# Optimization experiments

Measured on AMD Instinct MI355X. Metric: run time of the kernel, lower is better.

Reference implementation:

```python
import jax, jax.numpy as jnp
import numpy as np
from jax import lax

T = 512
CHUNK = 64
H = W = 28
C = 4
D_MODEL = H * W * C  # 3136
D_HIDDEN = 512
ALPHA = 0.9
ETA0 = 0.1
P = 2.0
EPS = 1e-6


def setup_inputs() -> dict:
    key = jax.random.key(0)
    ks = jax.random.split(key, 8)
    x = jax.random.normal(ks[0], (T, C, H, W), dtype=jnp.float32)
    conv_k_w = jax.random.normal(ks[1], (3, 3, C, C), dtype=jnp.float32) / 6.0  # lecun-ish: fan_in=36
    conv_v_w = jax.random.normal(ks[2], (3, 3, C, C), dtype=jnp.float32) / 6.0
    conv_k_b = jnp.zeros((C,), jnp.float32)
    conv_v_b = jnp.zeros((C,), jnp.float32)
    rms_k_scale = jnp.ones((C,), jnp.float32)
    rms_v_scale = jnp.ones((C,), jnp.float32)
    W1 = jax.random.normal(ks[3], (D_MODEL, D_HIDDEN), dtype=jnp.float32) / np.sqrt(D_MODEL).astype(np.float32)
    b1 = jnp.zeros((D_HIDDEN,), jnp.float32)
    W2 = jax.random.normal(ks[4], (D_HIDDEN, D_MODEL), dtype=jnp.float32) / np.sqrt(D_HIDDEN).astype(np.float32)
    b2 = jnp.zeros((D_MODEL,), jnp.float32)
    return {"x": x, "conv_k_w": conv_k_w, "conv_k_b": conv_k_b,
            "conv_v_w": conv_v_w, "conv_v_b": conv_v_b,
            "rms_k_scale": rms_k_scale, "rms_v_scale": rms_v_scale,
            "W1": W1, "b1": b1, "W2": W2, "b2": b2}


def _conv(x_nhwc, w, b):
    y = lax.conv_general_dilated(x_nhwc, w, window_strides=(1, 1), padding='SAME',
                                 dimension_numbers=('NHWC', 'HWIO', 'NHWC'))
    return y + b


def _rmsnorm(z, scale):
    inv = lax.rsqrt(jnp.mean(z * z, axis=-1, keepdims=True) + EPS)
    return z * inv * scale


def _mlp(params, k):
    w1, bb1, w2, bb2 = params
    return jax.nn.gelu(k @ w1 + bb1) @ w2 + bb2


def reference(x, conv_k_w, conv_k_b, conv_v_w, conv_v_b, rms_k_scale, rms_v_scale, W1, b1, W2, b2):
    t = x.shape[0]
    xh = jnp.transpose(x, (0, 2, 3, 1))  # [T,H,W,C]
    nk = _rmsnorm(_conv(xh, conv_k_w, conv_k_b), rms_k_scale).reshape(t, -1)  # [T, D_MODEL]
    nv = _rmsnorm(_conv(xh, conv_v_w, conv_v_b), rms_v_scale).reshape(t, -1)

    params0 = (W1, b1, W2, b2)

    def loss_per_token(params, k, v):
        pred = _mlp(params, k)
        return jnp.sum(jnp.abs(pred - v) ** P)

    etas = ETA0 * ALPHA ** jnp.arange(CHUNK, dtype=jnp.float32)
    betas = ALPHA ** jnp.arange(CHUNK, dtype=jnp.float32)
    weights = etas * (betas[-1] / betas)  # [CHUNK]

    n_chunks = t // CHUNK
    Kc = nk.reshape(n_chunks, CHUNK, D_MODEL)
    Vc = nv.reshape(n_chunks, CHUNK, D_MODEL)

    def chunk_body(params, kv):
        K, V = kv
        # per-token parameter grads: leaves have leading CHUNK axis
        grads = jax.vmap(jax.grad(loss_per_token), in_axes=(None, 0, 0))(params, K, V)
        new_params = jax.tree.map(
            lambda p, g: p - jnp.tensordot(weights, g, axes=((0,), (0,))), params, grads)
        Y = _mlp(new_params, K)  # recall on keys with updated fast weights
        return new_params, Y

    _, Y_chunks = lax.scan(chunk_body, params0, (Kc, Vc))
    Y = Y_chunks.reshape(t, D_MODEL)
    return Y.reshape(t, C, H, W)
```

## Files before the change

### kernel.cpp

```cpp
#include <hip/hip_runtime.h>
#include <math.h>

#define DM 3136
#define DH 512

typedef __attribute__((ext_vector_type(8))) short bf16x8;
typedef __attribute__((ext_vector_type(4))) float f32x4;

__device__ __forceinline__ ushort f2bf(float f) {
  union { float f; unsigned u; } v; v.f = f;
  unsigned r = v.u + 0x7FFFu + ((v.u >> 16) & 1u);
  return (ushort)(r >> 16);
}

#define MICRO_4x4 \
    acc[0][0] += a.x*b.x; acc[0][1] += a.x*b.y; acc[0][2] += a.x*b.z; acc[0][3] += a.x*b.w; \
    acc[1][0] += a.y*b.x; acc[1][1] += a.y*b.y; acc[1][2] += a.y*b.z; acc[1][3] += a.y*b.w; \
    acc[2][0] += a.z*b.x; acc[2][1] += a.z*b.y; acc[2][2] += a.z*b.z; acc[2][3] += a.z*b.w; \
    acc[3][0] += a.w*b.x; acc[3][1] += a.w*b.y; acc[3][2] += a.w*b.z; acc[3][3] += a.w*b.w;

__device__ __forceinline__ void gelu_both(float xx, float& g, float& gp) {
  const float c = 0.7978845608028654f;
  const float a = 0.044715f;
  float x2 = xx * xx;
  float u = c * (xx + a * xx * x2);
  float t = tanhf(u);
  g  = 0.5f * xx * (1.f + t);
  gp = 0.5f * (1.f + t) + 0.5f * xx * (1.f - t * t) * c * (1.f + 3.f * a * x2);
}
__device__ __forceinline__ float gelu_only(float xx) {
  const float c = 0.7978845608028654f;
  const float a = 0.044715f;
  float u = c * (xx + a * xx * xx * xx);
  return 0.5f * xx * (1.f + tanhf(u));
}

__device__ __forceinline__ void nt64_core(
    const ushort* __restrict__ A, int lda,
    const ushort* __restrict__ B, int ldb,
    int ksteps, f32x4* acc) {
  int lane = threadIdx.x & 63;
  int wv = threadIdx.x >> 6;
  int qr = wv >> 1, qc = wv & 1;
  int lr = lane & 15;
  int lk = (lane >> 4) << 3;
  const ushort* pa0 = A + (size_t)(qr * 32 + lr) * lda + lk;
  const ushort* pa1 = pa0 + (size_t)16 * lda;
  const ushort* pb0 = B + (size_t)(qc * 32 + lr) * ldb + lk;
  const ushort* pb1 = pb0 + (size_t)16 * ldb;
  bf16x8 a0 = *(const bf16x8*)pa0;
  bf16x8 a1 = *(const bf16x8*)pa1;
  bf16x8 b0 = *(const bf16x8*)pb0;
  bf16x8 b1 = *(const bf16x8*)pb1;
  for (int s = 0; s < ksteps; ++s) {
    int sn = (s + 1 < ksteps) ? (s + 1) * 32 : s * 32;
    bf16x8 na0 = *(const bf16x8*)(pa0 + sn);
    bf16x8 na1 = *(const bf16x8*)(pa1 + sn);
    bf16x8 nb0 = *(const bf16x8*)(pb0 + sn);
    bf16x8 nb1 = *(const bf16x8*)(pb1 + sn);
    acc[0] = __builtin_amdgcn_mfma_f32_16x16x32_bf16(a0, b0, acc[0], 0, 0, 0);
    acc[1] = __builtin_amdgcn_mfma_f32_16x16x32_bf16(a0, b1, acc[1], 0, 0, 0);
    acc[2] = __builtin_amdgcn_mfma_f32_16x16x32_bf16(a1, b0, acc[2], 0, 0, 0);
    acc[3] = __builtin_amdgcn_mfma_f32_16x16x32_bf16(a1, b1, acc[3], 0, 0, 0);
    a0 = na0; a1 = na1; b0 = nb0; b1 = nb1;
  }
}

__device__ __forceinline__ void nt64_store(const f32x4* acc, float* __restrict__ dst, int ldc) {
  int lane = threadIdx.x & 63, wv = threadIdx.x >> 6;
  int r0 = (wv >> 1) * 32 + ((lane >> 4) << 2);
  int c0 = (wv & 1) * 32 + (lane & 15);
  #pragma unroll
  for (int r = 0; r < 4; ++r) {
    dst[(size_t)(r0 + r) * ldc + c0]           = acc[0][r];
    dst[(size_t)(r0 + r) * ldc + c0 + 16]      = acc[1][r];
    dst[(size_t)(r0 + r + 16) * ldc + c0]      = acc[2][r];
    dst[(size_t)(r0 + r + 16) * ldc + c0 + 16] = acc[3][r];
  }
}

__global__ __launch_bounds__(256) void conv_rms(
    const float* __restrict__ x,
    const float* __restrict__ wk, const float* __restrict__ bk,
    const float* __restrict__ wv, const float* __restrict__ bv,
    const float* __restrict__ sk, const float* __restrict__ sv,
    const float* __restrict__ W1, ushort* __restrict__ w1tb,
    const float* __restrict__ W2, ushort* __restrict__ W2b0, ushort* __restrict__ W2tb0,
    ushort* __restrict__ nkb, float* __restrict__ nv) {
  __shared__ float smem[4160];
  int tid = threadIdx.x;
  if (blockIdx.x >= 1960) {
    int t = blockIdx.x - 1960;
    int d0 = (t % 49) * 64, h0 = (t / 49) * 64;
    int c = tid & 63, rq = tid >> 6;
    #pragma unroll
    for (int q = 0; q < 16; ++q) {
      int r = q * 4 + rq;
      float v = W2[(size_t)(h0 + r) * DM + d0 + c];
      smem[r * 65 + c] = v;
      W2b0[(size_t)(h0 + r) * DM + d0 + c] = f2bf(v);
    }
    __syncthreads();
    #pragma unroll
    for (int q = 0; q < 16; ++q) {
      int r = q * 4 + rq;
      W2tb0[(size_t)(d0 + r) * DH + h0 + c] = f2bf(smem[c * 65 + r]);
    }
    return;
  }
  if (blockIdx.x >= 1568) {
    int t = blockIdx.x - 1568;
    int d0 = (t % 49) * 64, h0 = (t / 49) * 64;
    int c = tid & 63, rq = tid >> 6;
    #pragma unroll
    for (int q = 0; q < 16; ++q) {
      int r = q * 4 + rq;
      smem[r * 65 + c] = W1[(size_t)(d0 + r) * 512 + h0 + c];
    }
    __syncthreads();
    #pragma unroll
    for (int q = 0; q < 16; ++q) {
      int r = q * 4 + rq;
      w1tb[(size_t)(h0 + r) * 3136 + d0 + c] = f2bf(smem[c * 65 + r]);
    }
    return;
  }
  float* swk = smem;
  float* swv = smem + 144;
  float* sb  = smem + 288;
  if (tid < 144) { swk[tid] = wk[tid]; swv[tid] = wv[tid]; }
  if (tid < 4) {
    sb[tid] = bk[tid]; sb[4 + tid] = bv[tid];
    sb[8 + tid] = sk[tid]; sb[12 + tid] = sv[tid];
  }
  __syncthreads();
  int idx = blockIdx.x * 256 + tid;
  int t = idx / 784, hw = idx - t * 784;
  int h = hw / 28, w = hw - h * 28;
  float ak[4], av[4];
  #pragma unroll
  for (int c = 0; c < 4; ++c) { ak[c] = sb[c]; av[c] = sb[4 + c]; }
  const float* xt = x + (size_t)t * DM;
  for (int kh = 0; kh < 3; ++kh) {
    int ih = h + kh - 1;
    if (ih < 0 || ih >= 28) continue;
    for (int kw = 0; kw < 3; ++kw) {
      int iw = w + kw - 1;
      if (iw < 0 || iw >= 28) continue;
      int base = (kh * 3 + kw) * 16;
      #pragma unroll
      for (int ci = 0; ci < 4; ++ci) {
        float xv = xt[ci * 784 + ih * 28 + iw];
        #pragma unroll
        for (int co = 0; co < 4; ++co) {
          ak[co] += xv * swk[base + ci * 4 + co];
          av[co] += xv * swv[base + ci * 4 + co];
        }
      }
    }
  }
  float mk = (ak[0]*ak[0] + ak[1]*ak[1] + ak[2]*ak[2] + ak[3]*ak[3]) * 0.25f + 1e-6f;
  float mv = (av[0]*av[0] + av[1]*av[1] + av[2]*av[2] + av[3]*av[3]) * 0.25f + 1e-6f;
  float ik = 1.f / sqrtf(mk), iv = 1.f / sqrtf(mv);
  ushort4 ok = { f2bf(ak[0]*ik*sb[8]), f2bf(ak[1]*ik*sb[9]),
                 f2bf(ak[2]*ik*sb[10]), f2bf(ak[3]*ik*sb[11]) };
  float4 ov = { av[0]*iv*sb[12], av[1]*iv*sb[13], av[2]*iv*sb[14], av[3]*iv*sb[15] };
  *(ushort4*)&nkb[(size_t)idx * 4] = ok;
  *(float4*)&nv[(size_t)idx * 4] = ov;
}

__global__ __launch_bounds__(256) void u1_kernel(
    const ushort* __restrict__ nkb, const ushort* __restrict__ w1tb,
    float* __restrict__ KKsl, float* __restrict__ Hb_sl) {
  f32x4 acc[4] = {{0.f,0.f,0.f,0.f},{0.f,0.f,0.f,0.f},{0.f,0.f,0.f,0.f},{0.f,0.f,0.f,0.f}};
  int job = blockIdx.x;
  if (job < 448) {
    int s = job % 7;
    int t = job / 7;
    int m0 = (t >> 3) * 64, n0 = (t & 7) * 64;
    nt64_core(nkb + (size_t)m0 * DM + s * 448, DM, w1tb + (size_t)n0 * DM + s * 448, DM, 14, acc);
    nt64_store(acc, Hb_sl + (size_t)s * 262144 + (size_t)m0 * 512 + n0, 512);
  } else {
    int j2 = job - 448;
    int p = j2 / 7, s = j2 % 7;
    int c = 0;
    while ((c + 1) * (c + 2) / 2 <= p) ++c;
    int j = p - c * (c + 1) / 2;
    nt64_core(nkb + (size_t)c * 64 * DM + s * 448, DM, nkb + (size_t)j * 64 * DM + s * 448, DM, 14, acc);
    nt64_store(acc, KKsl + ((size_t)p * 7 + s) * 4096, 64);
  }
}

__global__ __launch_bounds__(256) void u2_kernel(
    const float* __restrict__ KKsl, const float* __restrict__ Hb_sl,
    float* __restrict__ KKf, float* __restrict__ Hbase,
    const float* __restrict__ b1,
    float* __restrict__ Hh, ushort* __restrict__ Gb, ushort* __restrict__ Gtb,
    float* __restrict__ Gp) {
  int i = blockIdx.x * 256 + threadIdx.x;
  if (i < 147456) {
    int pair = i >> 12, e = i & 4095;
    float s = 0.f;
    #pragma unroll
    for (int t = 0; t < 7; ++t) s += KKsl[((size_t)pair * 7 + t) * 4096 + e];
    KKf[i] = s;
  } else {
    int j = i - 147456;
    float s = 0.f;
    #pragma unroll
    for (int t = 0; t < 7; ++t) s += Hb_sl[(size_t)t * 262144 + j];
    Hbase[j] = s;
    if (j < 32768) {
      Hh[j] = s;
      float g, gp;
      gelu_both(s + b1[j & 511], g, gp);
      Gb[j] = f2bf(g);
      Gtb[(j & 511) * 64 + (j >> 9)] = f2bf(g);
      Gp[j] = gp;
    }
  }
}

__device__ __forceinline__ void hred_body(
    int j, const float* __restrict__ Hb_c, const float* __restrict__ Hcorr, int nsl,
    const float* __restrict__ b1v,
    float* __restrict__ Hh, ushort* __restrict__ Gb, ushort* __restrict__ Gtb,
    float* __restrict__ Gp) {
  float s = Hb_c[j];
  for (int t = 0; t < nsl; ++t) s -= Hcorr[(size_t)t * 32768 + j];
  Hh[j] = s;
  float g, gp;
  gelu_both(s + b1v[j & 511], g, gp);
  Gb[j] = f2bf(g);
  Gtb[(j & 511) * 64 + (j >> 9)] = f2bf(g);
  Gp[j] = gp;
}

__device__ __forceinline__ void hs_corr_job(
    const float* __restrict__ KK, const float* __restrict__ Ewj,
    float* __restrict__ dst, int bx, float* smem) {
  float* As = smem;
  float* Bs = smem + 4096;
  int tid = threadIdx.x;
  int n0 = bx * 64;
  {
    int m = tid >> 2, ib = (tid & 3) * 16;
    #pragma unroll
    for (int q = 0; q < 4; ++q) {
      float4 v = *(const float4*)(KK + m * 64 + ib + q * 4);
      As[(ib + q*4 + 0)*64 + m] = v.x;
      As[(ib + q*4 + 1)*64 + m] = v.y;
      As[(ib + q*4 + 2)*64 + m] = v.z;
      As[(ib + q*4 + 3)*64 + m] = v.w;
    }
    int kr = tid >> 4, nn = (tid & 15) * 4;
    #pragma unroll
    for (int q = 0; q < 4; ++q)
      *(float4*)&Bs[(kr + q*16)*64 + nn] = *(const float4*)(Ewj + (size_t)(kr + q*16) * DH + n0 + nn);
  }
  __syncthreads();
  int tx = tid & 15, ty = tid >> 4;
  float acc[4][4] = {{0.f}};
  #pragma unroll 16
  for (int kk = 0; kk < 64; ++kk) {
    float4 a = *(const float4*)&As[kk*64 + ty * 4];
    float4 b = *(const float4*)&Bs[kk*64 + tx * 4];
    MICRO_4x4
  }
  #pragma unroll
  for (int r = 0; r < 4; ++r) {
    float4 v = { acc[r][0], acc[r][1], acc[r][2], acc[r][3] };
    *(float4*)&dst[(ty*4 + r) * DH + n0 + tx*4] = v;
  }
}

__global__ __launch_bounds__(256) void p4w2_kernel(
    const ushort* __restrict__ Dwb, const ushort* __restrict__ Dwtb,
    const ushort* __restrict__ Gtb, const ushort* __restrict__ W2b_c,
    const float* __restrict__ W2c, float* __restrict__ W2n,
    ushort* __restrict__ W2b_n, ushort* __restrict__ W2tb_n,
    float* __restrict__ Esl) {
  f32x4 acc[4] = {{0.f,0.f,0.f,0.f},{0.f,0.f,0.f,0.f},{0.f,0.f,0.f,0.f},{0.f,0.f,0.f,0.f}};
  int b = blockIdx.x;
  if (b < 56) {
    int s = b % 7, nt = b / 7;
    nt64_core(Dwb + s * 448, DM, W2b_c + (size_t)nt * 64 * DM + s * 448, DM, 14, acc);
    nt64_store(acc, Esl + (size_t)s * 32768 + nt * 64, 512);
  } else {
    int li = b - 56;
    int d0 = (li % 49) * 64, h0 = (li / 49) * 64;
    nt64_core(Gtb + (size_t)h0 * 64, 64, Dwtb + (size_t)d0 * 64, 64, 2, acc);
    int lane = threadIdx.x & 63, wvv = threadIdx.x >> 6;
    int r0 = (wvv >> 1) * 32 + ((lane >> 4) << 2);
    int c0 = (wvv & 1) * 32 + (lane & 15);
    #pragma unroll
    for (int r = 0; r < 4; ++r) {
      #pragma unroll
      for (int p = 0; p < 4; ++p) {
        int h = h0 + r0 + r + ((p >> 1) ? 16 : 0);
        int d = d0 + c0 + ((p & 1) ? 16 : 0);
        size_t off = (size_t)h * DM + d;
        float w = W2c[off] - acc[p][r];
        W2n[off] = w;
        ushort wb = f2bf(w);
        W2b_n[off] = wb;
        W2tb_n[(size_t)d * DH + h] = wb;
      }
    }
  }
}

__global__ __launch_bounds__(256) void g2h_kernel(
    const float* __restrict__ KKf, int ch,
    const float* __restrict__ Esl, const float* __restrict__ GpC,
    const float* __restrict__ Hcur, const float* __restrict__ b1e,
    float* __restrict__ b1o, ushort* __restrict__ G2b,
    float* __restrict__ EwOut, float* __restrict__ Hcorr) {
  __shared__ float smem[8192];
  int blk = blockIdx.x;
  int tid = threadIdx.x;
  int tri = ch * (ch + 1) / 2;
  if (blk < 32) {
    float* KKs = smem;
    float* Ews = smem + 4096;
    float* b1l = smem + 5120;
    const float* KKcc = KKf + (size_t)(tri + ch) * 4096;
    int n0 = blk * 16;
    #pragma unroll
    for (int q = 0; q < 4; ++q) {
      int e4 = q * 256 + tid;
      *(float4*)&KKs[e4 * 4] = *(const float4*)(KKcc + e4 * 4);
    }
    #pragma unroll
    for (int q = 0; q < 4; ++q) {
      int e = q * 256 + tid;
      int i = e >> 4, cc = e & 15;
      size_t off = (size_t)i * 512 + n0 + cc;
      float s = 0.f;
      #pragma unroll
      for (int sl = 0; sl < 7; ++sl) s += Esl[(size_t)sl * 32768 + off];
      Ews[e] = s * GpC[off];
    }
    __syncthreads();
    if (tid < 16) {
      float s = 0.f;
      for (int i = 0; i < 64; ++i) s += Ews[i * 16 + tid];
      b1l[tid] = b1e[n0 + tid] - s;
    }
    __syncthreads();
    #pragma unroll
    for (int q = 0; q < 4; ++q) {
      int e = q * 256 + tid;
      int mrow = e >> 4, cc = e & 15;
      float corr = 0.f;
      #pragma unroll 16
      for (int i = 0; i < 64; ++i) corr += KKs[mrow * 64 + i] * Ews[i * 16 + cc];
      float xx = Hcur[(size_t)mrow * 512 + n0 + cc] - corr + b1l[cc];
      G2b[(size_t)mrow * 512 + n0 + cc] = f2bf(gelu_only(xx));
    }
  } else {
    float* As = smem;
    float* Bs = smem + 4096;
    int bx = blk - 32;
    int n0 = bx * 64;
    #pragma unroll
    for (int q = 0; q < 16; ++q) {
      int e = q * 256 + tid;
      int k = e >> 6, c = e & 63;
      size_t off = (size_t)k * 512 + n0 + c;
      float s = 0.f;
      #pragma unroll
      for (int sl = 0; sl < 7; ++sl) s += Esl[(size_t)sl * 32768 + off];
      float ew = s * GpC[off];
      Bs[k * 64 + c] = ew;
      EwOut[off] = ew;
    }
    {
      const float* KK = KKf + (size_t)((ch + 1) * (ch + 2) / 2 + ch) * 4096;
      int m = tid >> 2, ib = (tid & 3) * 16;
      #pragma unroll
      for (int q = 0; q < 4; ++q) {
        float4 v = *(const float4*)(KK + m * 64 + ib + q * 4);
        As[(ib + q*4 + 0)*64 + m] = v.x;
        As[(ib + q*4 + 1)*64 + m] = v.y;
        As[(ib + q*4 + 2)*64 + m] = v.z;
        As[(ib + q*4 + 3)*64 + m] = v.w;
      }
    }
    __syncthreads();
    if (tid < 64) {
      float s = 0.f;
      for (int k = 0; k < 64; ++k) s += Bs[k * 64 + tid];
      b1o[n0 + tid] = b1e[n0 + tid] - s;
    }
    int tx = tid & 15, ty = tid >> 4;
    float acc[4][4] = {{0.f}};
    #pragma unroll 16
    for (int kk = 0; kk < 64; ++kk) {
      float4 a = *(const float4*)&As[kk*64 + ty * 4];
      float4 b = *(const float4*)&Bs[kk*64 + tx * 4];
      MICRO_4x4
    }
    float* dst = Hcorr + (size_t)ch * 32768;
    #pragma unroll
    for (int r = 0; r < 4; ++r) {
      float4 v = { acc[r][0], acc[r][1], acc[r][2], acc[r][3] };
      *(float4*)&dst[(ty*4 + r) * DH + n0 + tx*4] = v;
    }
  }
}

__global__ __launch_bounds__(256) void p7h_kernel(
    const ushort* __restrict__ G2b, const ushort* __restrict__ W2tb,
    const float* __restrict__ b2n, float* __restrict__ out, int t0,
    const float* __restrict__ Hbase_n, const float* __restrict__ Hcorr, int nsl,
    const float* __restrict__ b1n,
    float* __restrict__ Hh, ushort* __restrict__ Gb_n, ushort* __restrict__ Gtb_n,
    float* __restrict__ Gp) {
  int b = blockIdx.x;
  if (b < 49) {
    f32x4 acc[4] = {{0.f,0.f,0.f,0.f},{0.f,0.f,0.f,0.f},{0.f,0.f,0.f,0.f},{0.f,0.f,0.f,0.f}};
    int n0 = b * 64;
    nt64_core(G2b, 512, W2tb + (size_t)n0 * 512, 512, 16, acc);
    int lane = threadIdx.x & 63, wvv = threadIdx.x >> 6;
    int r0 = (wvv >> 1) * 32 + ((lane >> 4) << 2);
    int c0 = (wvv & 1) * 32 + (lane & 15);
    #pragma unroll
    for (int r = 0; r < 4; ++r) {
      #pragma unroll
      for (int p = 0; p < 4; ++p) {
        int m = r0 + r + ((p >> 1) ? 16 : 0);
        int d = n0 + c0 + ((p & 1) ? 16 : 0);
        out[(size_t)(t0 + m) * DM + d] = acc[p][r] + b2n[d];
      }
    }
  } else {
    int j = (b - 49) * 256 + threadIdx.x;
    hred_body(j, Hbase_n, Hcorr, nsl, b1n, Hh, Gb_n, Gtb_n, Gp);
  }
}

__global__ __launch_bounds__(256) void p3d_kernel(
    const ushort* __restrict__ Gnb, const ushort* __restrict__ W2tb,
    const float* __restrict__ Vn, const float* __restrict__ b2in, float wc2,
    float* __restrict__ b2out, ushort* __restrict__ Dwb, ushort* __restrict__ Dwtb,
    const float* __restrict__ KKf, int ch,
    const float* __restrict__ Ewst, float* __restrict__ Hcorr) {
  __shared__ float smem[8192];
  int blk = blockIdx.x;
  if (blk < 49) {
    f32x4 acc[4] = {{0.f,0.f,0.f,0.f},{0.f,0.f,0.f,0.f},{0.f,0.f,0.f,0.f},{0.f,0.f,0.f,0.f}};
    int n0 = blk * 64;
    nt64_core(Gnb, 512, W2tb + (size_t)n0 * 512, 512, 16, acc);
    int lane = threadIdx.x & 63, wvv = threadIdx.x >> 6;
    int qr = wvv >> 1, qc = wvv & 1;
    int r0 = qr * 32 + ((lane >> 4) << 2);
    int c0 = qc * 32 + (lane & 15);
    float csum[2] = {0.f, 0.f};
    #pragma unroll
    for (int r = 0; r < 4; ++r) {
      #pragma unroll
      for (int p = 0; p < 4; ++p) {
        int m = r0 + r + ((p >> 1) ? 16 : 0);
        int dl = c0 + ((p & 1) ? 16 : 0);
        int d = n0 + dl;
        float dw = wc2 * (acc[p][r] + b2in[d] - Vn[(size_t)m * DM + d]);
        ushort db = f2bf(dw);
        Dwb[(size_t)m * DM + d] = db;
        Dwtb[(size_t)d * 64 + m] = db;
        csum[p & 1] += dw;
      }
    }
    int slot = qr * 4 + ((lane >> 4) & 3);
    smem[(size_t)c0 * 8 + slot] = csum[0];
    smem[(size_t)(c0 + 16) * 8 + slot] = csum[1];
    __syncthreads();
    if (threadIdx.x < 64) {
      float s = 0.f;
      #pragma unroll
      for (int q = 0; q < 8; ++q) s += smem[threadIdx.x * 8 + q];
      b2out[n0 + threadIdx.x] = b2in[n0 + threadIdx.x] - s;
    }
  } else {
    int j2 = blk - 49;
    int j = j2 >> 3, bx = j2 & 7;
    int trin = (ch + 2) * (ch + 3) / 2;
    hs_corr_job(KKf + (size_t)(trin + j) * 4096, Ewst + (size_t)j * 32768,
                Hcorr + (size_t)j * 32768, bx, smem);
  }
}

extern "C" void kernel_launch(void* const* d_in, const int* in_sizes, int n_in,
                              void* d_out, int out_size, void* d_ws, size_t ws_size,
                              hipStream_t stream) {
  const float* x  = (const float*)d_in[0];
  const float* wk = (const float*)d_in[1];
  const float* bk = (const float*)d_in[2];
  const float* wv = (const float*)d_in[3];
  const float* bv = (const float*)d_in[4];
  const float* sk = (const float*)d_in[5];
  const float* sv = (const float*)d_in[6];
  const float* W1 = (const float*)d_in[7];
  const float* b1 = (const float*)d_in[8];
  const float* W2 = (const float*)d_in[9];
  const float* b2 = (const float*)d_in[10];
  float* out = (float*)d_out;
  float* ws  = (float*)d_ws;

  ushort* nkb   = (ushort*)ws;
  ushort* w1tb  = (ushort*)(ws + 802816);
  float* nv     = ws + 1605632;
  float* W2A    = nv + 1605632;
  float* W2B    = W2A + 1605632;
  float* bf_base = W2B + 1605632;
  ushort* W2b0  = (ushort*)bf_base;
  ushort* W2tb0 = (ushort*)(bf_base + 802816);
  ushort* W2bA  = (ushort*)(bf_base + 1605632);
  ushort* W2bB  = (ushort*)(bf_base + 2408448);
  ushort* W2tbA = (ushort*)(bf_base + 3211264);
  ushort* W2tbB = (ushort*)(bf_base + 4014080);
  float* Esl    = bf_base + 4816896;
  float* Hb_sl  = Esl + 229376;
  float* KKsl   = Hb_sl + 1835008;
  float* Hbase  = KKsl + 1032192;
  float* KKf    = Hbase + 262144;
  float* HhA    = KKf + 147456;
  float* HhB    = HhA + 32768;
  float* GpA    = HhB + 32768;
  float* GpB    = GpA + 32768;
  ushort* GbA   = (ushort*)(GpB + 32768);
  ushort* GbB   = (ushort*)(GpB + 49152);
  ushort* GtbA  = (ushort*)(GpB + 65536);
  ushort* GtbB  = (ushort*)(GpB + 81920);
  ushort* G2b   = (ushort*)(GpB + 98304);
  ushort* Dwb   = (ushort*)(GpB + 114688);
  ushort* Dwtb  = (ushort*)(GpB + 215040);
  float* Ewst   = GpB + 315392;
  float* Hcorr  = Ewst + 262144;
  float* b1A    = Hcorr + 229376;
  float* b1B    = b1A + 512;
  float* b2A    = b1B + 512;
  float* b2B    = b2A + 3136;

  float* W2buf[2]   = { W2A, W2B };
  ushort* W2bb[2]   = { W2bA, W2bB };
  ushort* W2tbb[2]  = { W2tbA, W2tbB };
  ushort* Gbb[2]    = { GbA, GbB };
  ushort* Gtbb[2]   = { GtbA, GtbB };
  float* Hhb[2]     = { HhA, HhB };
  float* Gpb[2]     = { GpA, GpB };
  float* b1buf[2]   = { b1A, b1B };
  float* b2buf[2]   = { b2A, b2B };

  float wc2 = 2.0f * (float)(0.1 * pow(0.9, 63.0));

  conv_rms<<<2352, 256, 0, stream>>>(x, wk, bk, wv, bv, sk, sv,
                                     W1, w1tb, W2, W2b0, W2tb0, nkb, nv);
  u1_kernel<<<700, 256, 0, stream>>>(nkb, w1tb, KKsl, Hb_sl);
  u2_kernel<<<1600, 256, 0, stream>>>(KKsl, Hb_sl, KKf, Hbase, b1, HhA, GbA, GtbA, GpA);
  p3d_kernel<<<49, 256, 0, stream>>>(GbA, W2tb0, nv, b2, wc2, b2A, Dwb, Dwtb,
                                     KKf, 0, Ewst, Hcorr);

  for (int ch = 0; ch < 8; ++ch) {
    const float* b1e  = ch ? b1buf[(ch - 1) & 1] : b1;
    const float* W2c  = ch ? W2buf[(ch - 1) & 1] : W2;
    const ushort* W2b_c = ch ? W2bb[(ch - 1) & 1] : W2b0;

    p4w2_kernel<<<448, 256, 0, stream>>>(
        Dwb, Dwtb, Gtbb[ch & 1], W2b_c, W2c,
        W2buf[ch & 1], W2bb[ch & 1], W2tbb[ch & 1], Esl);
    g2h_kernel<<<32 + (ch < 7 ? 8 : 0), 256, 0, stream>>>(
        KKf, ch, Esl, Gpb[ch & 1], Hhb[ch & 1], b1e, b1buf[ch & 1],
        G2b, Ewst + (size_t)ch * 32768, Hcorr);
    p7h_kernel<<<49 + (ch < 7 ? 128 : 0), 256, 0, stream>>>(
        G2b, W2tbb[ch & 1], b2buf[ch & 1], out, ch * 64,
        Hbase + (size_t)((ch + 1) & 7) * 32768, Hcorr, ch + 1, b1buf[ch & 1],
        Hhb[(ch + 1) & 1], Gbb[(ch + 1) & 1], Gtbb[(ch + 1) & 1], Gpb[(ch + 1) & 1]);
    if (ch < 7) {
      int gF = 49 + (ch < 6 ? 8 * (ch + 1) : 0);
      p3d_kernel<<<gF, 256, 0, stream>>>(
          Gbb[(ch + 1) & 1], W2tbb[ch & 1], nv + (size_t)(ch + 1) * 200704,
          b2buf[ch & 1], wc2, b2buf[(ch + 1) & 1], Dwb, Dwtb,
          KKf, ch, Ewst, Hcorr);
    }
  }
}
```

Before: 418.2 us.

## Split K across two wave groups in the 64-column GEMM kernels

The p3d and p7h GEMM paths move to 512-thread blocks. Each 256-thread group computes half of the K=512 reduction, and the two partial results are summed through shared memory, so each block runs more waves to cover latency on a grid of only 49 tiles. A dedicated pred0 kernel replaces the first p3d launch. g2h pads its KK shared tile to a stride of 65 to avoid bank conflicts, and the hred part of p7h now uses 512 threads per block. The cost is an extra shared-memory reduction and barrier, and half of each block sits idle during the epilogue.

```diff
diff --git a/kernel.cpp b/kernel.cpp
--- a/kernel.cpp
+++ b/kernel.cpp
@@ -66,6 +66,58 @@
   }
 }
 
+__device__ __forceinline__ void nt64_group(
+    const ushort* __restrict__ A, int lda,
+    const ushort* __restrict__ B, int ldb,
+    int k0, int ksteps, int lane, int wv, f32x4* acc) {
+  int qr = wv >> 1, qc = wv & 1;
+  int lr = lane & 15;
+  int lk = (lane >> 4) << 3;
+  const ushort* pa0 = A + (size_t)(qr * 32 + lr) * lda + k0 + lk;
+  const ushort* pa1 = pa0 + (size_t)16 * lda;
+  const ushort* pb0 = B + (size_t)(qc * 32 + lr) * ldb + k0 + lk;
+  const ushort* pb1 = pb0 + (size_t)16 * ldb;
+  bf16x8 a0 = *(const bf16x8*)pa0;
+  bf16x8 a1 = *(const bf16x8*)pa1;
+  bf16x8 b0 = *(const bf16x8*)pb0;
+  bf16x8 b1 = *(const bf16x8*)pb1;
+  for (int s = 0; s < ksteps; ++s) {
+    int sn = (s + 1 < ksteps) ? (s + 1) * 32 : s * 32;
+    bf16x8 na0 = *(const bf16x8*)(pa0 + sn);
+    bf16x8 na1 = *(const bf16x8*)(pa1 + sn);
+    bf16x8 nb0 = *(const bf16x8*)(pb0 + sn);
+    bf16x8 nb1 = *(const bf16x8*)(pb1 + sn);
+    acc[0] = __builtin_amdgcn_mfma_f32_16x16x32_bf16(a0, b0, acc[0], 0, 0, 0);
+    acc[1] = __builtin_amdgcn_mfma_f32_16x16x32_bf16(a0, b1, acc[1], 0, 0, 0);
+    acc[2] = __builtin_amdgcn_mfma_f32_16x16x32_bf16(a1, b0, acc[2], 0, 0, 0);
+    acc[3] = __builtin_amdgcn_mfma_f32_16x16x32_bf16(a1, b1, acc[3], 0, 0, 0);
+    a0 = na0; a1 = na1; b0 = nb0; b1 = nb1;
+  }
+}
+
+__device__ __forceinline__ void ksplit_reduce(
+    f32x4* acc, float* red, int grp, int lane, int wv) {
+  int r0 = (wv >> 1) * 32 + ((lane >> 4) << 2);
+  int c0 = (wv & 1) * 32 + (lane & 15);
+  if (grp == 1) {
+    #pragma unroll
+    for (int r = 0; r < 4; ++r) {
+      #pragma unroll
+      for (int p = 0; p < 4; ++p)
+        red[(r0 + r + ((p >> 1) ? 16 : 0)) * 64 + c0 + ((p & 1) ? 16 : 0)] = acc[p][r];
+    }
+  }
+  __syncthreads();
+  if (grp == 0) {
+    #pragma unroll
+    for (int r = 0; r < 4; ++r) {
+      #pragma unroll
+      for (int p = 0; p < 4; ++p)
+        acc[p][r] += red[(r0 + r + ((p >> 1) ? 16 : 0)) * 64 + c0 + ((p & 1) ? 16 : 0)];
+    }
+  }
+}
+
 __device__ __forceinline__ void nt64_store(const f32x4* acc, float* __restrict__ dst, int ldc) {
   int lane = threadIdx.x & 63, wv = threadIdx.x >> 6;
   int r0 = (wv >> 1) * 32 + ((lane >> 4) << 2);
@@ -76,6 +128,44 @@
     dst[(size_t)(r0 + r) * ldc + c0 + 16]      = acc[1][r];
     dst[(size_t)(r0 + r + 16) * ldc + c0]      = acc[2][r];
     dst[(size_t)(r0 + r + 16) * ldc + c0 + 16] = acc[3][r];
+  }
+}
+
+__device__ __forceinline__ void dw_epilogue512(
+    const f32x4* acc, int n0, const float* __restrict__ Vn,
+    const float* __restrict__ b2in, float wc2,
+    ushort* __restrict__ Dwb_o, ushort* __restrict__ Dwt_o,
+    float* __restrict__ b2out, float* smem, int tid) {
+  if (tid < 256) {
+    int lane = tid & 63, wvv = tid >> 6;
+    int qr = wvv >> 1, qc = wvv & 1;
+    int r0 = qr * 32 + ((lane >> 4) << 2);
+    int c0 = qc * 32 + (lane & 15);
+    float csum[2] = {0.f, 0.f};
+    #pragma unroll
+    for (int r = 0; r < 4; ++r) {
+      #pragma unroll
+      for (int p = 0; p < 4; ++p) {
+        int m = r0 + r + ((p >> 1) ? 16 : 0);
+        int dl = c0 + ((p & 1) ? 16 : 0);
+        int d = n0 + dl;
+        float dw = wc2 * (acc[p][r] + b2in[d] - Vn[(size_t)m * DM + d]);
+        ushort db = f2bf(dw);
+        Dwb_o[(size_t)m * DM + d] = db;
+        Dwt_o[(size_t)d * 64 + m] = db;
+        csum[p & 1] += dw;
+      }
+    }
+    int slot = qr * 4 + ((lane >> 4) & 3);
+    smem[(size_t)c0 * 8 + slot] = csum[0];
+    smem[(size_t)(c0 + 16) * 8 + slot] = csum[1];
+  }
+  __syncthreads();
+  if (tid < 64) {
+    float s = 0.f;
+    #pragma unroll
+    for (int q = 0; q < 8; ++q) s += smem[tid * 8 + q];
+    b2out[n0 + tid] = b2in[n0 + tid] - s;
   }
 }
 
@@ -236,29 +326,28 @@
   Gp[j] = gp;
 }
 
-__device__ __forceinline__ void hs_corr_job(
+__device__ __forceinline__ void hs_corr_load(
     const float* __restrict__ KK, const float* __restrict__ Ewj,
-    float* __restrict__ dst, int bx, float* smem) {
-  float* As = smem;
-  float* Bs = smem + 4096;
-  int tid = threadIdx.x;
+    int bx, float* As, float* Bs, int tid) {
   int n0 = bx * 64;
-  {
-    int m = tid >> 2, ib = (tid & 3) * 16;
-    #pragma unroll
-    for (int q = 0; q < 4; ++q) {
-      float4 v = *(const float4*)(KK + m * 64 + ib + q * 4);
-      As[(ib + q*4 + 0)*64 + m] = v.x;
-      As[(ib + q*4 + 1)*64 + m] = v.y;
-      As[(ib + q*4 + 2)*64 + m] = v.z;
-      As[(ib + q*4 + 3)*64 + m] = v.w;
-    }
-    int kr = tid >> 4, nn = (tid & 15) * 4;
-    #pragma unroll
-    for (int q = 0; q < 4; ++q)
-      *(float4*)&Bs[(kr + q*16)*64 + nn] = *(const float4*)(Ewj + (size_t)(kr + q*16) * DH + n0 + nn);
-  }
-  __syncthreads();
+  int m = tid >> 2, ib = (tid & 3) * 16;
+  #pragma unroll
+  for (int q = 0; q < 4; ++q) {
+    float4 v = *(const float4*)(KK + m * 64 + ib + q * 4);
+    As[(ib + q*4 + 0)*64 + m] = v.x;
+    As[(ib + q*4 + 1)*64 + m] = v.y;
+    As[(ib + q*4 + 2)*64 + m] = v.z;
+    As[(ib + q*4 + 3)*64 + m] = v.w;
+  }
+  int kr = tid >> 4, nn = (tid & 15) * 4;
+  #pragma unroll
+  for (int q = 0; q < 4; ++q)
+    *(float4*)&Bs[(kr + q*16)*64 + nn] = *(const float4*)(Ewj + (size_t)(kr + q*16) * DH + n0 + nn);
+}
+
+__device__ __forceinline__ void hs_corr_compute(
+    const float* As, const float* Bs, float* __restrict__ dst, int bx, int tid) {
+  int n0 = bx * 64;
   int tx = tid & 15, ty = tid >> 4;
   float acc[4][4] = {{0.f}};
   #pragma unroll 16
@@ -272,6 +361,21 @@
     float4 v = { acc[r][0], acc[r][1], acc[r][2], acc[r][3] };
     *(float4*)&dst[(ty*4 + r) * DH + n0 + tx*4] = v;
   }
+}
+
+__global__ __launch_bounds__(512) void pred0_kernel(
+    const ushort* __restrict__ Gb0, const ushort* __restrict__ W2tb0,
+    const float* __restrict__ V, const float* __restrict__ b2in, float wc2,
+    float* __restrict__ b2out, ushort* __restrict__ Dwb_o, ushort* __restrict__ Dwt_o) {
+  __shared__ float smem[4608];
+  f32x4 acc[4] = {{0.f,0.f,0.f,0.f},{0.f,0.f,0.f,0.f},{0.f,0.f,0.f,0.f},{0.f,0.f,0.f,0.f}};
+  int tid = threadIdx.x;
+  int grp = tid >> 8, lane = tid & 63, wvv = (tid >> 6) & 3;
+  int n0 = blockIdx.x * 64;
+  nt64_group(Gb0, 512, W2tb0 + (size_t)n0 * 512, 512, grp * 256, 8, lane, wvv, acc);
+  ksplit_reduce(acc, smem, grp, lane, wvv);
+  __syncthreads();
+  dw_epilogue512(acc, n0, V, b2in, wc2, Dwb_o, Dwt_o, b2out, smem + 4096, tid);
 }
 
 __global__ __launch_bounds__(256) void p4w2_kernel(
@@ -316,20 +420,20 @@
     const float* __restrict__ Hcur, const float* __restrict__ b1e,
     float* __restrict__ b1o, ushort* __restrict__ G2b,
     float* __restrict__ EwOut, float* __restrict__ Hcorr) {
-  __shared__ float smem[8192];
+  __shared__ float smem[8320];
   int blk = blockIdx.x;
   int tid = threadIdx.x;
   int tri = ch * (ch + 1) / 2;
   if (blk < 32) {
     float* KKs = smem;
-    float* Ews = smem + 4096;
-    float* b1l = smem + 5120;
+    float* Ews = smem + 4160;
+    float* b1l = smem + 5184;
     const float* KKcc = KKf + (size_t)(tri + ch) * 4096;
     int n0 = blk * 16;
     #pragma unroll
-    for (int q = 0; q < 4; ++q) {
-      int e4 = q * 256 + tid;
-      *(float4*)&KKs[e4 * 4] = *(const float4*)(KKcc + e4 * 4);
+    for (int q = 0; q < 16; ++q) {
+      int e = q * 256 + tid;
+      KKs[(e >> 6) * 65 + (e & 63)] = KKcc[e];
     }
     #pragma unroll
     for (int q = 0; q < 4; ++q) {
@@ -354,7 +458,7 @@
       int mrow = e >> 4, cc = e & 15;
       float corr = 0.f;
       #pragma unroll 16
-      for (int i = 0; i < 64; ++i) corr += KKs[mrow * 64 + i] * Ews[i * 16 + cc];
+      for (int i = 0; i < 64; ++i) corr += KKs[mrow * 65 + i] * Ews[i * 16 + cc];
       float xx = Hcur[(size_t)mrow * 512 + n0 + cc] - corr + b1l[cc];
       G2b[(size_t)mrow * 512 + n0 + cc] = f2bf(gelu_only(xx));
     }
@@ -410,37 +514,42 @@
   }
 }
 
-__global__ __launch_bounds__(256) void p7h_kernel(
+__global__ __launch_bounds__(512) void p7h_kernel(
     const ushort* __restrict__ G2b, const ushort* __restrict__ W2tb,
     const float* __restrict__ b2n, float* __restrict__ out, int t0,
     const float* __restrict__ Hbase_n, const float* __restrict__ Hcorr, int nsl,
     const float* __restrict__ b1n,
     float* __restrict__ Hh, ushort* __restrict__ Gb_n, ushort* __restrict__ Gtb_n,
     float* __restrict__ Gp) {
+  __shared__ float red[4096];
   int b = blockIdx.x;
+  int tid = threadIdx.x;
   if (b < 49) {
     f32x4 acc[4] = {{0.f,0.f,0.f,0.f},{0.f,0.f,0.f,0.f},{0.f,0.f,0.f,0.f},{0.f,0.f,0.f,0.f}};
+    int grp = tid >> 8, lane = tid & 63, wvv = (tid >> 6) & 3;
     int n0 = b * 64;
-    nt64_core(G2b, 512, W2tb + (size_t)n0 * 512, 512, 16, acc);
-    int lane = threadIdx.x & 63, wvv = threadIdx.x >> 6;
-    int r0 = (wvv >> 1) * 32 + ((lane >> 4) << 2);
-    int c0 = (wvv & 1) * 32 + (lane & 15);
-    #pragma unroll
-    for (int r = 0; r < 4; ++r) {
-      #pragma unroll
-      for (int p = 0; p < 4; ++p) {
-        int m = r0 + r + ((p >> 1) ? 16 : 0);
-        int d = n0 + c0 + ((p & 1) ? 16 : 0);
-        out[(size_t)(t0 + m) * DM + d] = acc[p][r] + b2n[d];
+    nt64_group(G2b, 512, W2tb + (size_t)n0 * 512, 512, grp * 256, 8, lane, wvv, acc);
+    ksplit_reduce(acc, red, grp, lane, wvv);
+    if (grp == 0) {
+      int r0 = (wvv >> 1) * 32 + ((lane >> 4) << 2);
+      int c0 = (wvv & 1) * 32 + (lane & 15);
+      #pragma unroll
+      for (int r = 0; r < 4; ++r) {
+        #pragma unroll
+        for (int p = 0; p < 4; ++p) {
+          int m = r0 + r + ((p >> 1) ? 16 : 0);
+          int d = n0 + c0 + ((p & 1) ? 16 : 0);
+          out[(size_t)(t0 + m) * DM + d] = acc[p][r] + b2n[d];
+        }
       }
     }
   } else {
-    int j = (b - 49) * 256 + threadIdx.x;
+    int j = (b - 49) * 512 + tid;
     hred_body(j, Hbase_n, Hcorr, nsl, b1n, Hh, Gb_n, Gtb_n, Gp);
   }
 }
 
-__global__ __launch_bounds__(256) void p3d_kernel(
+__global__ __launch_bounds__(512) void p3d_kernel(
     const ushort* __restrict__ Gnb, const ushort* __restrict__ W2tb,
     const float* __restrict__ Vn, const float* __restrict__ b2in, float wc2,
     float* __restrict__ b2out, ushort* __restrict__ Dwb, ushort* __restrict__ Dwtb,
@@ -448,45 +557,25 @@
     const float* __restrict__ Ewst, float* __restrict__ Hcorr) {
   __shared__ float smem[8192];
   int blk = blockIdx.x;
+  int tid = threadIdx.x;
   if (blk < 49) {
     f32x4 acc[4] = {{0.f,0.f,0.f,0.f},{0.f,0.f,0.f,0.f},{0.f,0.f,0.f,0.f},{0.f,0.f,0.f,0.f}};
+    int grp = tid >> 8, lane = tid & 63, wvv = (tid >> 6) & 3;
     int n0 = blk * 64;
-    nt64_core(Gnb, 512, W2tb + (size_t)n0 * 512, 512, 16, acc);
-    int lane = threadIdx.x & 63, wvv = threadIdx.x >> 6;
-    int qr = wvv >> 1, qc = wvv & 1;
-    int r0 = qr * 32 + ((lane >> 4) << 2);
-    int c0 = qc * 32 + (lane & 15);
-    float csum[2] = {0.f, 0.f};
-    #pragma unroll
-    for (int r = 0; r < 4; ++r) {
-      #pragma unroll
-      for (int p = 0; p < 4; ++p) {
-        int m = r0 + r + ((p >> 1) ? 16 : 0);
-        int dl = c0 + ((p & 1) ? 16 : 0);
-        int d = n0 + dl;
-        float dw = wc2 * (acc[p][r] + b2in[d] - Vn[(size_t)m * DM + d]);
-        ushort db = f2bf(dw);
-        Dwb[(size_t)m * DM + d] = db;
-        Dwtb[(size_t)d * 64 + m] = db;
-        csum[p & 1] += dw;
-      }
-    }
-    int slot = qr * 4 + ((lane >> 4) & 3);
-    smem[(size_t)c0 * 8 + slot] = csum[0];
-    smem[(size_t)(c0 + 16) * 8 + slot] = csum[1];
+    nt64_group(Gnb, 512, W2tb + (size_t)n0 * 512, 512, grp * 256, 8, lane, wvv, acc);
+    ksplit_reduce(acc, smem, grp, lane, wvv);
     __syncthreads();
-    if (threadIdx.x < 64) {
-      float s = 0.f;
-      #pragma unroll
-      for (int q = 0; q < 8; ++q) s += smem[threadIdx.x * 8 + q];
-      b2out[n0 + threadIdx.x] = b2in[n0 + threadIdx.x] - s;
-    }
+    dw_epilogue512(acc, n0, Vn, b2in, wc2, Dwb, Dwtb, b2out, smem + 4096, tid);
   } else {
     int j2 = blk - 49;
     int j = j2 >> 3, bx = j2 & 7;
     int trin = (ch + 2) * (ch + 3) / 2;
-    hs_corr_job(KKf + (size_t)(trin + j) * 4096, Ewst + (size_t)j * 32768,
-                Hcorr + (size_t)j * 32768, bx, smem);
+    const float* KK = KKf + (size_t)(trin + j) * 4096;
+    const float* Ewj = Ewst + (size_t)j * 32768;
+    float* dst = Hcorr + (size_t)j * 32768;
+    if (tid < 256) hs_corr_load(KK, Ewj, bx, smem, smem + 4096, tid);
+    __syncthreads();
+    if (tid < 256) hs_corr_compute(smem, smem + 4096, dst, bx, tid);
   }
 }
 
@@ -558,8 +647,7 @@
                                      W1, w1tb, W2, W2b0, W2tb0, nkb, nv);
   u1_kernel<<<700, 256, 0, stream>>>(nkb, w1tb, KKsl, Hb_sl);
   u2_kernel<<<1600, 256, 0, stream>>>(KKsl, Hb_sl, KKf, Hbase, b1, HhA, GbA, GtbA, GpA);
-  p3d_kernel<<<49, 256, 0, stream>>>(GbA, W2tb0, nv, b2, wc2, b2A, Dwb, Dwtb,
-                                     KKf, 0, Ewst, Hcorr);
+  pred0_kernel<<<49, 512, 0, stream>>>(GbA, W2tb0, nv, b2, wc2, b2A, Dwb, Dwtb);
 
   for (int ch = 0; ch < 8; ++ch) {
     const float* b1e  = ch ? b1buf[(ch - 1) & 1] : b1;
@@ -572,13 +660,13 @@
     g2h_kernel<<<32 + (ch < 7 ? 8 : 0), 256, 0, stream>>>(
         KKf, ch, Esl, Gpb[ch & 1], Hhb[ch & 1], b1e, b1buf[ch & 1],
         G2b, Ewst + (size_t)ch * 32768, Hcorr);
-    p7h_kernel<<<49 + (ch < 7 ? 128 : 0), 256, 0, stream>>>(
+    p7h_kernel<<<49 + (ch < 7 ? 64 : 0), 512, 0, stream>>>(
         G2b, W2tbb[ch & 1], b2buf[ch & 1], out, ch * 64,
         Hbase + (size_t)((ch + 1) & 7) * 32768, Hcorr, ch + 1, b1buf[ch & 1],
         Hhb[(ch + 1) & 1], Gbb[(ch + 1) & 1], Gtbb[(ch + 1) & 1], Gpb[(ch + 1) & 1]);
     if (ch < 7) {
       int gF = 49 + (ch < 6 ? 8 * (ch + 1) : 0);
-      p3d_kernel<<<gF, 256, 0, stream>>>(
+      p3d_kernel<<<gF, 512, 0, stream>>>(
           Gbb[(ch + 1) & 1], W2tbb[ch & 1], nv + (size_t)(ch + 1) * 200704,
           b2buf[ch & 1], wc2, b2buf[(ch + 1) & 1], Dwb, Dwtb,
           KKf, ch, Ewst, Hcorr);
```

After: 441.0 us. 5.4% more time.

## Fuse next-chunk hidden reduction into g2h and merge p7h with p3d

Applied to the files above, without the earlier changes.

The next chunk's hidden-state correction (KK×Ew) is now computed inline in g2hr blocks, together with the Hcorr reduction and GELU. Previously it was a separate matmul written to Hcorr and then reduced in p7h. The recall output and the next chunk's prediction/Dw epilogue now share one kernel (yp3), removing one launch per chunk and a global round trip of the Hcorr slice. KK shared tiles are padded to a stride of 65 to avoid bank conflicts. In exchange, g2hr recomputes the Esl reduction in 128 extra blocks, and the work across dependent stages is rebalanced.

```diff
diff --git a/kernel.cpp b/kernel.cpp
--- a/kernel.cpp
+++ b/kernel.cpp
@@ -79,6 +79,42 @@
   }
 }
 
+__device__ __forceinline__ void dw_epilogue256(
+    const f32x4* acc, int n0, const float* __restrict__ Vn,
+    const float* __restrict__ b2in, float wc2,
+    ushort* __restrict__ Dwb_o, ushort* __restrict__ Dwt_o,
+    float* __restrict__ b2out, float* smem) {
+  int lane = threadIdx.x & 63, wvv = threadIdx.x >> 6;
+  int qr = wvv >> 1, qc = wvv & 1;
+  int r0 = qr * 32 + ((lane >> 4) << 2);
+  int c0 = qc * 32 + (lane & 15);
+  float csum[2] = {0.f, 0.f};
+  #pragma unroll
+  for (int r = 0; r < 4; ++r) {
+    #pragma unroll
+    for (int p = 0; p < 4; ++p) {
+      int m = r0 + r + ((p >> 1) ? 16 : 0);
+      int dl = c0 + ((p & 1) ? 16 : 0);
+      int d = n0 + dl;
+      float dw = wc2 * (acc[p][r] + b2in[d] - Vn[(size_t)m * DM + d]);
+      ushort db = f2bf(dw);
+      Dwb_o[(size_t)m * DM + d] = db;
+      Dwt_o[(size_t)d * 64 + m] = db;
+      csum[p & 1] += dw;
+    }
+  }
+  int slot = qr * 4 + ((lane >> 4) & 3);
+  smem[(size_t)c0 * 8 + slot] = csum[0];
+  smem[(size_t)(c0 + 16) * 8 + slot] = csum[1];
+  __syncthreads();
+  if (threadIdx.x < 64) {
+    float s = 0.f;
+    #pragma unroll
+    for (int q = 0; q < 8; ++q) s += smem[threadIdx.x * 8 + q];
+    b2out[n0 + threadIdx.x] = b2in[n0 + threadIdx.x] - s;
+  }
+}
+
 __global__ __launch_bounds__(256) void conv_rms(
     const float* __restrict__ x,
     const float* __restrict__ wk, const float* __restrict__ bk,
@@ -221,21 +257,6 @@
   }
 }
 
-__device__ __forceinline__ void hred_body(
-    int j, const float* __restrict__ Hb_c, const float* __restrict__ Hcorr, int nsl,
-    const float* __restrict__ b1v,
-    float* __restrict__ Hh, ushort* __restrict__ Gb, ushort* __restrict__ Gtb,
-    float* __restrict__ Gp) {
-  float s = Hb_c[j];
-  for (int t = 0; t < nsl; ++t) s -= Hcorr[(size_t)t * 32768 + j];
-  Hh[j] = s;
-  float g, gp;
-  gelu_both(s + b1v[j & 511], g, gp);
-  Gb[j] = f2bf(g);
-  Gtb[(j & 511) * 64 + (j >> 9)] = f2bf(g);
-  Gp[j] = gp;
-}
-
 __device__ __forceinline__ void hs_corr_job(
     const float* __restrict__ KK, const float* __restrict__ Ewj,
     float* __restrict__ dst, int bx, float* smem) {
@@ -272,6 +293,17 @@
     float4 v = { acc[r][0], acc[r][1], acc[r][2], acc[r][3] };
     *(float4*)&dst[(ty*4 + r) * DH + n0 + tx*4] = v;
   }
+}
+
+__global__ __launch_bounds__(256) void pred0_kernel(
+    const ushort* __restrict__ Gb0, const ushort* __restrict__ W2tb0,
+    const float* __restrict__ V, const float* __restrict__ b2in, float wc2,
+    float* __restrict__ b2out, ushort* __restrict__ Dwb_o, ushort* __restrict__ Dwt_o) {
+  __shared__ float smem[512];
+  f32x4 acc[4] = {{0.f,0.f,0.f,0.f},{0.f,0.f,0.f,0.f},{0.f,0.f,0.f,0.f},{0.f,0.f,0.f,0.f}};
+  int n0 = blockIdx.x * 64;
+  nt64_core(Gb0, 512, W2tb0 + (size_t)n0 * 512, 512, 16, acc);
+  dw_epilogue256(acc, n0, V, b2in, wc2, Dwb_o, Dwt_o, b2out, smem);
 }
 
 __global__ __launch_bounds__(256) void p4w2_kernel(
@@ -310,26 +342,28 @@
   }
 }
 
-__global__ __launch_bounds__(256) void g2h_kernel(
+__global__ __launch_bounds__(256) void g2hr_kernel(
     const float* __restrict__ KKf, int ch,
     const float* __restrict__ Esl, const float* __restrict__ GpC,
     const float* __restrict__ Hcur, const float* __restrict__ b1e,
-    float* __restrict__ b1o, ushort* __restrict__ G2b,
-    float* __restrict__ EwOut, float* __restrict__ Hcorr) {
-  __shared__ float smem[8192];
+    float* __restrict__ b1o, ushort* __restrict__ G2b, float* __restrict__ EwOut,
+    const float* __restrict__ Hcorr, const float* __restrict__ Hbase_n,
+    float* __restrict__ HhN, ushort* __restrict__ GbN,
+    ushort* __restrict__ GtbN, float* __restrict__ GpN) {
+  __shared__ float smem[5200];
   int blk = blockIdx.x;
   int tid = threadIdx.x;
   int tri = ch * (ch + 1) / 2;
   if (blk < 32) {
     float* KKs = smem;
-    float* Ews = smem + 4096;
-    float* b1l = smem + 5120;
+    float* Ews = smem + 4160;
+    float* b1l = smem + 5184;
     const float* KKcc = KKf + (size_t)(tri + ch) * 4096;
     int n0 = blk * 16;
     #pragma unroll
-    for (int q = 0; q < 4; ++q) {
-      int e4 = q * 256 + tid;
-      *(float4*)&KKs[e4 * 4] = *(const float4*)(KKcc + e4 * 4);
+    for (int q = 0; q < 16; ++q) {
+      int e = q * 256 + tid;
+      KKs[(e >> 6) * 65 + (e & 63)] = KKcc[e];
     }
     #pragma unroll
     for (int q = 0; q < 4; ++q) {
@@ -354,13 +388,12 @@
       int mrow = e >> 4, cc = e & 15;
       float corr = 0.f;
       #pragma unroll 16
-      for (int i = 0; i < 64; ++i) corr += KKs[mrow * 64 + i] * Ews[i * 16 + cc];
+      for (int i = 0; i < 64; ++i) corr += KKs[mrow * 65 + i] * Ews[i * 16 + cc];
       float xx = Hcur[(size_t)mrow * 512 + n0 + cc] - corr + b1l[cc];
       G2b[(size_t)mrow * 512 + n0 + cc] = f2bf(gelu_only(xx));
     }
-  } else {
-    float* As = smem;
-    float* Bs = smem + 4096;
+  } else if (blk < 40) {
+    float* Bs = smem;
     int bx = blk - 32;
     int n0 = bx * 64;
     #pragma unroll
@@ -375,48 +408,68 @@
       Bs[k * 64 + c] = ew;
       EwOut[off] = ew;
     }
-    {
-      const float* KK = KKf + (size_t)((ch + 1) * (ch + 2) / 2 + ch) * 4096;
-      int m = tid >> 2, ib = (tid & 3) * 16;
-      #pragma unroll
-      for (int q = 0; q < 4; ++q) {
-        float4 v = *(const float4*)(KK + m * 64 + ib + q * 4);
-        As[(ib + q*4 + 0)*64 + m] = v.x;
-        As[(ib + q*4 + 1)*64 + m] = v.y;
-        As[(ib + q*4 + 2)*64 + m] = v.z;
-        As[(ib + q*4 + 3)*64 + m] = v.w;
-      }
-    }
     __syncthreads();
     if (tid < 64) {
       float s = 0.f;
       for (int k = 0; k < 64; ++k) s += Bs[k * 64 + tid];
       b1o[n0 + tid] = b1e[n0 + tid] - s;
     }
-    int tx = tid & 15, ty = tid >> 4;
-    float acc[4][4] = {{0.f}};
+  } else {
+    float* Ewt = smem;
+    float* KKs = smem + 1024;
+    float* b1l = smem + 2064;
+    int bh = blk - 40;
+    int m0 = (bh >> 5) * 16;
+    int c0 = (bh & 31) * 16;
+    #pragma unroll
+    for (int q = 0; q < 4; ++q) {
+      int e = q * 256 + tid;
+      int i = e >> 4, cl = e & 15;
+      size_t off = (size_t)i * 512 + c0 + cl;
+      float s = 0.f;
+      #pragma unroll
+      for (int sl = 0; sl < 7; ++sl) s += Esl[(size_t)sl * 32768 + off];
+      Ewt[i * 16 + cl] = s * GpC[off];
+    }
+    const float* KK = KKf + (size_t)((ch + 1) * (ch + 2) / 2 + ch) * 4096;
+    #pragma unroll
+    for (int q = 0; q < 4; ++q) {
+      int e = q * 256 + tid;
+      int ml = e >> 6, i = e & 63;
+      KKs[ml * 65 + i] = KK[(m0 + ml) * 64 + i];
+    }
+    __syncthreads();
+    if (tid < 16) {
+      float s = 0.f;
+      for (int i = 0; i < 64; ++i) s += Ewt[i * 16 + tid];
+      b1l[tid] = b1e[c0 + tid] - s;
+    }
+    __syncthreads();
+    int ml = tid >> 4, cl = tid & 15;
+    int m = m0 + ml, c = c0 + cl;
+    float corr = 0.f;
     #pragma unroll 16
-    for (int kk = 0; kk < 64; ++kk) {
-      float4 a = *(const float4*)&As[kk*64 + ty * 4];
-      float4 b = *(const float4*)&Bs[kk*64 + tx * 4];
-      MICRO_4x4
-    }
-    float* dst = Hcorr + (size_t)ch * 32768;
-    #pragma unroll
-    for (int r = 0; r < 4; ++r) {
-      float4 v = { acc[r][0], acc[r][1], acc[r][2], acc[r][3] };
-      *(float4*)&dst[(ty*4 + r) * DH + n0 + tx*4] = v;
-    }
-  }
-}
-
-__global__ __launch_bounds__(256) void p7h_kernel(
+    for (int i = 0; i < 64; ++i) corr += KKs[ml * 65 + i] * Ewt[i * 16 + cl];
+    size_t off = (size_t)m * 512 + c;
+    float s = Hbase_n[off] - corr;
+    for (int j = 0; j < ch; ++j) s -= Hcorr[(size_t)j * 32768 + off];
+    HhN[off] = s;
+    float g, gp;
+    gelu_both(s + b1l[cl], g, gp);
+    GbN[off] = f2bf(g);
+    GtbN[(size_t)c * 64 + m] = f2bf(g);
+    GpN[off] = gp;
+  }
+}
+
+__global__ __launch_bounds__(256) void yp3_kernel(
     const ushort* __restrict__ G2b, const ushort* __restrict__ W2tb,
     const float* __restrict__ b2n, float* __restrict__ out, int t0,
-    const float* __restrict__ Hbase_n, const float* __restrict__ Hcorr, int nsl,
-    const float* __restrict__ b1n,
-    float* __restrict__ Hh, ushort* __restrict__ Gb_n, ushort* __restrict__ Gtb_n,
-    float* __restrict__ Gp) {
+    const ushort* __restrict__ Gnb, const float* __restrict__ Vn, float wc2,
+    float* __restrict__ b2out, ushort* __restrict__ Dwb, ushort* __restrict__ Dwtb,
+    const float* __restrict__ KKf, int ch,
+    const float* __restrict__ Ewst, float* __restrict__ Hcorr) {
+  __shared__ float smem[8192];
   int b = blockIdx.x;
   if (b < 49) {
     f32x4 acc[4] = {{0.f,0.f,0.f,0.f},{0.f,0.f,0.f,0.f},{0.f,0.f,0.f,0.f},{0.f,0.f,0.f,0.f}};
@@ -434,55 +487,13 @@
         out[(size_t)(t0 + m) * DM + d] = acc[p][r] + b2n[d];
       }
     }
+  } else if (ch < 7 && b < 98) {
+    f32x4 acc[4] = {{0.f,0.f,0.f,0.f},{0.f,0.f,0.f,0.f},{0.f,0.f,0.f,0.f},{0.f,0.f,0.f,0.f}};
+    int n0 = (b - 49) * 64;
+    nt64_core(Gnb, 512, W2tb + (size_t)n0 * 512, 512, 16, acc);
+    dw_epilogue256(acc, n0, Vn, b2n, wc2, Dwb, Dwtb, b2out, smem);
   } else {
-    int j = (b - 49) * 256 + threadIdx.x;
-    hred_body(j, Hbase_n, Hcorr, nsl, b1n, Hh, Gb_n, Gtb_n, Gp);
-  }
-}
-
-__global__ __launch_bounds__(256) void p3d_kernel(
-    const ushort* __restrict__ Gnb, const ushort* __restrict__ W2tb,
-    const float* __restrict__ Vn, const float* __restrict__ b2in, float wc2,
-    float* __restrict__ b2out, ushort* __restrict__ Dwb, ushort* __restrict__ Dwtb,
-    const float* __restrict__ KKf, int ch,
-    const float* __restrict__ Ewst, float* __restrict__ Hcorr) {
-  __shared__ float smem[8192];
-  int blk = blockIdx.x;
-  if (blk < 49) {
-    f32x4 acc[4] = {{0.f,0.f,0.f,0.f},{0.f,0.f,0.f,0.f},{0.f,0.f,0.f,0.f},{0.f,0.f,0.f,0.f}};
-    int n0 = blk * 64;
-    nt64_core(Gnb, 512, W2tb + (size_t)n0 * 512, 512, 16, acc);
-    int lane = threadIdx.x & 63, wvv = threadIdx.x >> 6;
-    int qr = wvv >> 1, qc = wvv & 1;
-    int r0 = qr * 32 + ((lane >> 4) << 2);
-    int c0 = qc * 32 + (lane & 15);
-    float csum[2] = {0.f, 0.f};
-    #pragma unroll
-    for (int r = 0; r < 4; ++r) {
-      #pragma unroll
-      for (int p = 0; p < 4; ++p) {
-        int m = r0 + r + ((p >> 1) ? 16 : 0);
-        int dl = c0 + ((p & 1) ? 16 : 0);
-        int d = n0 + dl;
-        float dw = wc2 * (acc[p][r] + b2in[d] - Vn[(size_t)m * DM + d]);
-        ushort db = f2bf(dw);
-        Dwb[(size_t)m * DM + d] = db;
-        Dwtb[(size_t)d * 64 + m] = db;
-        csum[p & 1] += dw;
-      }
-    }
-    int slot = qr * 4 + ((lane >> 4) & 3);
-    smem[(size_t)c0 * 8 + slot] = csum[0];
-    smem[(size_t)(c0 + 16) * 8 + slot] = csum[1];
-    __syncthreads();
-    if (threadIdx.x < 64) {
-      float s = 0.f;
-      #pragma unroll
-      for (int q = 0; q < 8; ++q) s += smem[threadIdx.x * 8 + q];
-      b2out[n0 + threadIdx.x] = b2in[n0 + threadIdx.x] - s;
-    }
-  } else {
-    int j2 = blk - 49;
+    int j2 = b - (ch < 7 ? 98 : 49);
     int j = j2 >> 3, bx = j2 & 7;
     int trin = (ch + 2) * (ch + 3) / 2;
     hs_corr_job(KKf + (size_t)(trin + j) * 4096, Ewst + (size_t)j * 32768,
@@ -558,8 +569,7 @@
                                      W1, w1tb, W2, W2b0, W2tb0, nkb, nv);
   u1_kernel<<<700, 256, 0, stream>>>(nkb, w1tb, KKsl, Hb_sl);
   u2_kernel<<<1600, 256, 0, stream>>>(KKsl, Hb_sl, KKf, Hbase, b1, HhA, GbA, GtbA, GpA);
-  p3d_kernel<<<49, 256, 0, stream>>>(GbA, W2tb0, nv, b2, wc2, b2A, Dwb, Dwtb,
-                                     KKf, 0, Ewst, Hcorr);
+  pred0_kernel<<<49, 256, 0, stream>>>(GbA, W2tb0, nv, b2, wc2, b2A, Dwb, Dwtb);
 
   for (int ch = 0; ch < 8; ++ch) {
     const float* b1e  = ch ? b1buf[(ch - 1) & 1] : b1;
@@ -569,19 +579,16 @@
     p4w2_kernel<<<448, 256, 0, stream>>>(
         Dwb, Dwtb, Gtbb[ch & 1], W2b_c, W2c,
         W2buf[ch & 1], W2bb[ch & 1], W2tbb[ch & 1], Esl);
-    g2h_kernel<<<32 + (ch < 7 ? 8 : 0), 256, 0, stream>>>(
+    g2hr_kernel<<<(ch < 7 ? 168 : 32), 256, 0, stream>>>(
         KKf, ch, Esl, Gpb[ch & 1], Hhb[ch & 1], b1e, b1buf[ch & 1],
-        G2b, Ewst + (size_t)ch * 32768, Hcorr);
-    p7h_kernel<<<49 + (ch < 7 ? 128 : 0), 256, 0, stream>>>(
+        G2b, Ewst + (size_t)ch * 32768,
+        Hcorr, Hbase + (size_t)((ch + 1) & 7) * 32768,
+        Hhb[(ch + 1) & 1], Gbb[(ch + 1) & 1], Gtbb[(ch + 1) & 1], Gpb[(ch + 1) & 1]);
+    int g3 = 49 + (ch < 7 ? 49 : 0) + (ch < 6 ? 8 * (ch + 1) : 0);
+    yp3_kernel<<<g3, 256, 0, stream>>>(
         G2b, W2tbb[ch & 1], b2buf[ch & 1], out, ch * 64,
-        Hbase + (size_t)((ch + 1) & 7) * 32768, Hcorr, ch + 1, b1buf[ch & 1],
-        Hhb[(ch + 1) & 1], Gbb[(ch + 1) & 1], Gtbb[(ch + 1) & 1], Gpb[(ch + 1) & 1]);
-    if (ch < 7) {
-      int gF = 49 + (ch < 6 ? 8 * (ch + 1) : 0);
-      p3d_kernel<<<gF, 256, 0, stream>>>(
-          Gbb[(ch + 1) & 1], W2tbb[ch & 1], nv + (size_t)(ch + 1) * 200704,
-          b2buf[ch & 1], wc2, b2buf[(ch + 1) & 1], Dwb, Dwtb,
-          KKf, ch, Ewst, Hcorr);
-    }
-  }
-}
+        Gbb[(ch + 1) & 1], nv + (size_t)((ch + 1) & 7) * 200704, wc2,
+        b2buf[(ch + 1) & 1], Dwb, Dwtb,
+        KKf, ch, Ewst, Hcorr);
+  }
+}
```

Result: faster. 352.6 us (-15.7%).
